# Kernel tuning notes

Hardware: AMD Instinct MI355X
Metric: run time of the kernel (lower is better)

## Reference

```python
import jax, jax.numpy as jnp
import numpy as np

B, N, D, Q, H = 8, 2048, 64, 16, 2
C = 2 * D + 1          # combined dim = 129
C8 = C // 8            # per-head qk dim = 16
K = 8192               # number of observed nodes
NEG = -9.0e15


def setup_inputs() -> dict:
    key = jax.random.key(0)
    ks = jax.random.split(key, 18)
    s = 0.05
    inp = {
        "x": jax.random.normal(ks[0], (B, N, D + 1), jnp.float32),
        "h": jax.random.normal(ks[1], (B, N, D), jnp.float32),
        "query_vectors": jax.random.normal(ks[2], (K, Q), jnp.float32),
        "adj": jax.random.randint(ks[3], (B, N, N), 0, 2, jnp.int32),
        "nodes_flat": jnp.arange(K, dtype=jnp.int32),
        # per-head attention projections (jax convention: x @ W + b)
        "Wq": jax.random.normal(ks[4], (H, C, C8), jnp.float32) * s,
        "bq": jax.random.normal(ks[5], (H, C8), jnp.float32) * s,
        "Wk": jax.random.normal(ks[6], (H, C, C8), jnp.float32) * s,
        "bk": jax.random.normal(ks[7], (H, C8), jnp.float32) * s,
        "Wv": jax.random.normal(ks[8], (H, C, C), jnp.float32) * s,
        "bv": jax.random.normal(ks[9], (H, C), jnp.float32) * s,
        # hypernetwork MLP_Param weights for reset / update / candidate gates
        "W_r": jax.random.normal(ks[10], (Q, C, D), jnp.float32) * s,
        "b_r": jax.random.normal(ks[11], (Q, D), jnp.float32) * s,
        "W_u": jax.random.normal(ks[12], (Q, C, D), jnp.float32) * s,
        "b_u": jax.random.normal(ks[13], (Q, D), jnp.float32) * s,
        "W_c": jax.random.normal(ks[14], (Q, C, D), jnp.float32) * s,
        "b_c": jax.random.normal(ks[15], (Q, D), jnp.float32) * s,
    }
    return inp


def _gate(x_sel, qv, W, b):
    # MLP_Param: W_n = einsum('nd,dio->nio', qv, W); out = x @ W_n + qv @ b
    # contract the combined dim first to avoid the [K, C, D] intermediate
    t = jnp.einsum('kc,qco->kqo', x_sel, W)      # [K, Q, D]
    return jnp.einsum('kq,kqo->ko', qv, t) + qv @ b


def reference(x, h, query_vectors, adj, nodes_flat,
              Wq, bq, Wk, bk, Wv, bv,
              W_r, b_r, W_u, b_u, W_c, b_c):
    combined = jnp.concatenate([x, h], axis=-1)                 # [B, N, C]
    q = jnp.einsum('bnc,hcd->hbnd', combined, Wq) + bq[:, None, None, :]
    k = jnp.einsum('bnc,hcd->hbnd', combined, Wk) + bk[:, None, None, :]
    v = jnp.einsum('bnc,hcd->hbnd', combined, Wv) + bv[:, None, None, :]
    scores = jnp.einsum('hbnd,hbmd->hbnm', q, k) / jnp.sqrt(jnp.float32(C8))
    scores = jax.nn.leaky_relu(scores, 0.2)
    scores = jnp.where(adj[None] == 0, NEG, scores)
    attn = jax.nn.softmax(scores, axis=-1)                      # [H, B, N, N]
    h_prime = jnp.einsum('hbnm,hbmc->hbnc', attn, v)
    comb_attn = h_prime.mean(axis=0)                            # [B, N, C]

    sel = comb_attn.reshape(-1, C)[nodes_flat]                  # [K, C]
    r = jax.nn.sigmoid(_gate(sel, query_vectors, W_r, b_r))     # [K, D]
    u = jax.nn.sigmoid(_gate(sel, query_vectors, W_u, b_u))     # [K, D]

    h_flat = h.reshape(-1, D)
    h_sel = r * h_flat[nodes_flat]                              # r * h[nodes_ind]
    h_flat = h_flat.at[nodes_flat].set(h_sel)
    h_new = h_flat.reshape(h.shape)

    comb_new = jnp.concatenate([x, h_new], axis=-1)             # [B, N, C]
    sel2 = comb_new.reshape(-1, C)[nodes_flat]
    cand = jnp.tanh(_gate(sel2, query_vectors, W_c, b_c))       # [K, D]

    return (1.0 - u) * h_sel + u * cand                         # [K, D]
```

## Files before the change

### kernel.cpp

```cpp
#include <hip/hip_runtime.h>
#include <hip/hip_bf16.h>


typedef _Float16 h2_t __attribute__((ext_vector_type(2)));
typedef _Float16 h8_t __attribute__((ext_vector_type(8)));
typedef float    f4_t __attribute__((ext_vector_type(4)));
#define MFMA16x32(a,b,c) __builtin_amdgcn_mfma_f32_16x16x32_f16(a,b,c,0,0,0)

#define OB_QG    0
#define OB_KG    524288
#define OB_VT    1048576
#define OB_MASK  5767168
#define OB_WALL  7864320
#define OB_HACC  7971840
#define OB_LSUM  16622592
#define OB_WTRU  16688128
#define OB_WTC   17253376

__global__ __launch_bounds__(256) void pack_adj(const int* __restrict__ adj,
                                                unsigned* __restrict__ mask) {
    long tg = (long)blockIdx.x * 256 + threadIdx.x;
    for (int it = 0; it < 32; ++it) {
        long i = tg + (long)it * 524288;
        int a = adj[i];
        unsigned long long bal = __ballot(a != 0);
        if ((threadIdx.x & 63) == 0)
            *(unsigned long long*)(mask + (i >> 5)) = bal;
    }
}

__global__ __launch_bounds__(256) void repack_all(
    const float* __restrict__ Wq, const float* __restrict__ bq,
    const float* __restrict__ Wk, const float* __restrict__ bk,
    const float* __restrict__ Wv, const float* __restrict__ bv,
    const float* __restrict__ Wr, const float* __restrict__ br,
    const float* __restrict__ Wu, const float* __restrict__ bu,
    const float* __restrict__ Wc, const float* __restrict__ bc,
    _Float16* __restrict__ Wall, _Float16* __restrict__ WtRu,
    _Float16* __restrict__ WtC) {
    int idx = blockIdx.x * 256 + threadIdx.x;
    if (idx < 6720) {
        int ct = idx / 320;
        int rem = idx % 320;
        int s = rem >> 6, lane = rem & 63;
        int n = ct * 16 + (lane & 15);
        int quad = lane >> 4;
        int h2 = (n >= 164) ? 1 : 0;
        int nn = n - h2 * 164;
        h8_t v;
        #pragma unroll
        for (int j = 0; j < 8; ++j) {
            int k = s * 32 + quad * 8 + j;
            float f = 0.f;
            if (n < 328) {
                if (nn < 16) {
                    if (k < 129)       f = Wq[(h2 * 129 + k) * 16 + nn];
                    else if (k == 129) f = bq[h2 * 16 + nn];
                } else if (nn < 32) {
                    int d = nn - 16;
                    if (k < 129)       f = Wk[(h2 * 129 + k) * 16 + d];
                    else if (k == 129) f = bk[h2 * 16 + d];
                } else {
                    int vc = nn - 32;
                    if (vc < 129) {
                        if (k < 129)       f = Wv[(h2 * 129 + k) * 129 + vc];
                        else if (k == 129) f = bv[h2 * 129 + vc];
                    }
                }
            }
            v[j] = (_Float16)f;
        }
        *(h8_t*)(Wall + (size_t)idx * 8) = v;
    } else if (idx < 6720 + 35328) {
        int i2 = idx - 6720;
        int s = i2 / 512;
        int rem = i2 % 512;
        int ct = rem >> 6, lane = rem & 63;
        int o = ct * 16 + (lane & 15);
        int quad = lane >> 4;
        const float* W = (o < 64) ? Wr : Wu;
        const float* bb = (o < 64) ? br : bu;
        int oc = o & 63;
        h8_t v;
        #pragma unroll
        for (int j = 0; j < 8; ++j) {
            int kk = s * 32 + quad * 8 + j;
            float f = 0.f;
            if (kk < 2176) {
                int q = kk / 136, c = kk % 136;
                if (c < 129) f = W[(q * 129 + c) * 64 + oc];
            } else if (kk < 2192) {
                f = bb[(kk - 2176) * 64 + oc];
            }
            v[j] = (_Float16)f;
        }
        *(h8_t*)(WtRu + (size_t)i2 * 8) = v;
    } else if (idx < 59712) {
        int i2 = idx - 6720 - 35328;
        int s = i2 / 256;
        int rem = i2 % 256;
        int ct = rem >> 6, lane = rem & 63;
        int o = ct * 16 + (lane & 15);
        int quad = lane >> 4;
        h8_t v;
        #pragma unroll
        for (int j = 0; j < 8; ++j) {
            int kk = s * 32 + quad * 8 + j;
            float f = 0.f;
            if (kk < 2176) {
                int q = kk / 136, c = kk % 136;
                if (c < 129) f = Wc[(q * 129 + c) * 64 + o];
            } else if (kk < 2192) {
                f = bc[(kk - 2176) * 64 + o];
            }
            v[j] = (_Float16)f;
        }
        *(h8_t*)(WtC + (size_t)i2 * 8) = v;
    }
}

__global__ __launch_bounds__(256) void qkv_mfma(
    const float* __restrict__ x, const float* __restrict__ h,
    const _Float16* __restrict__ Wall,
    _Float16* __restrict__ qg, _Float16* __restrict__ kg,
    _Float16* __restrict__ vT) {
    __shared__ _Float16 at[16 * 168];
    __shared__ _Float16 vls[264 * 16];
    int t = threadIdx.x;
    int row0 = blockIdx.x * 16;
    for (int idx = t; idx < 16 * 160; idx += 256) {
        int r = idx / 160, c = idx % 160;
        int grow = row0 + r;
        float v = 0.f;
        if (c < 65)       v = x[grow * 65 + c];
        else if (c < 129) v = h[grow * 64 + (c - 65)];
        else if (c == 129) v = 1.0f;
        at[r * 168 + c] = (_Float16)v;
    }
    __syncthreads();
    int lane = t & 63, w = t >> 6;
    int l16 = lane & 15, quad = lane >> 4;
    for (int ct = w; ct < 21; ct += 4) {
        f4_t acc; acc[0]=0.f; acc[1]=0.f; acc[2]=0.f; acc[3]=0.f;
        int n = ct * 16 + l16;
        const _Float16* wp = Wall + ((size_t)ct * 320 + lane) * 8;
        #pragma unroll
        for (int s = 0; s < 5; ++s) {
            h8_t a = *(const h8_t*)(at + l16 * 168 + s * 32 + quad * 8);
            h8_t b = *(const h8_t*)(wp + (size_t)s * 512);
            acc = MFMA16x32(a, b, acc);
        }
        if (n < 328) {
            int h2 = (n >= 164) ? 1 : 0;
            int nn = n - h2 * 164;
            #pragma unroll
            for (int r = 0; r < 4; ++r) {
                int row = quad * 4 + r;
                _Float16 v = (_Float16)acc[r];
                if (nn < 16)      qg[(h2 * 8192 + row0 + row) * 16 + nn] = v;
                else if (nn < 32) kg[(h2 * 8192 + row0 + row) * 16 + (nn - 16)] = v;
                else              vls[(h2 * 132 + (nn - 32)) * 16 + row] = v;
            }
        }
    }
    __syncthreads();
    for (int idx = t; idx < 528; idx += 256) {
        int col = idx >> 1, half = idx & 1;
        int h2 = (col >= 132) ? 1 : 0;
        int cc = col - h2 * 132;
        uint4 v = ((const uint4*)vls)[idx];
        *(uint4*)(vT + ((size_t)(h2 * 144 + cc)) * 8192 + row0 + half * 8) = v;
    }
}

__global__ __launch_bounds__(256) void attn_fused(
    const _Float16* __restrict__ qg, const _Float16* __restrict__ kg,
    const _Float16* __restrict__ vT, const unsigned* __restrict__ mask,
    float* __restrict__ hacc, float* __restrict__ lsum, int tps) {
    __shared__ _Float16 vsm[144 * 88];
    __shared__ _Float16 pT[4 * 16 * 88];
    int t = threadIdx.x;
    int pid = blockIdx.x + 32 * (blockIdx.y + 8 * blockIdx.z);
    int xcd = pid & 7, j = pid >> 3;
    int nt = j & 31, hb = xcd, sp = j >> 5;
    int h2 = hb >> 2, b = hb & 3;
    int base = h2 * 8192 + b * 2048;
    int n0 = nt * 64;
    int lane = t & 63, w = t >> 6;
    int l16 = lane & 15, q = lane >> 4;
    int qrow = n0 + w * 16 + l16;
    _Float16* pTw = pT + w * 16 * 88;
    h8_t zero8;
    #pragma unroll
    for (int i = 0; i < 8; ++i) zero8[i] = (_Float16)0.f;
    h8_t qf = zero8;
    if (q < 2) qf = *(const h8_t*)(qg + (base + qrow) * 16 + 8 * q);
    const unsigned* mrw = mask + (b * 2048 + qrow) * 64;
    f4_t acc[9];
    #pragma unroll
    for (int i = 0; i < 9; ++i) { acc[i][0]=0.f; acc[i][1]=0.f; acc[i][2]=0.f; acc[i][3]=0.f; }
    float l_run = 0.f;

    int c0 = t >> 3, ch0 = t & 7;
    const _Float16* vsrc = vT + ((size_t)h2 * 144) * 8192 + b * 2048 + ch0 * 8;
    int mt0 = sp * tps, mtE = sp * tps + tps;

    uint4 rv0, rv1, rv2, rv3, rv4;
    h8_t kpre[4];
    uint2 mpre;
    {
        int m0 = mt0 * 64;
        rv0 = *(const uint4*)(vsrc + (size_t)(c0      ) * 8192 + m0);
        rv1 = *(const uint4*)(vsrc + (size_t)(c0 + 32 ) * 8192 + m0);
        rv2 = *(const uint4*)(vsrc + (size_t)(c0 + 64 ) * 8192 + m0);
        rv3 = *(const uint4*)(vsrc + (size_t)(c0 + 96 ) * 8192 + m0);
        if (t < 128) rv4 = *(const uint4*)(vsrc + (size_t)(c0 + 128) * 8192 + m0);
        #pragma unroll
        for (int ct = 0; ct < 4; ++ct) {
            kpre[ct] = zero8;
            if (q < 2)
                kpre[ct] = *(const h8_t*)(kg + (base + m0 + 16 * ct + l16) * 16 + 8 * q);
        }
        mpre = *(const uint2*)(mrw + (m0 >> 5));
    }

    for (int mt = mt0; mt < mtE; ++mt) {
        int m0 = mt * 64;
        __syncthreads();
        *(uint4*)(vsm + (c0      ) * 88 + ch0 * 8) = rv0;
        *(uint4*)(vsm + (c0 + 32 ) * 88 + ch0 * 8) = rv1;
        *(uint4*)(vsm + (c0 + 64 ) * 88 + ch0 * 8) = rv2;
        *(uint4*)(vsm + (c0 + 96 ) * 88 + ch0 * 8) = rv3;
        if (t < 128) *(uint4*)(vsm + (c0 + 128) * 88 + ch0 * 8) = rv4;
        __syncthreads();
        h8_t kf[4];
        #pragma unroll
        for (int ct = 0; ct < 4; ++ct) kf[ct] = kpre[ct];
        uint2 mw = mpre;
        if (mt + 1 < mtE) {
            int m1 = m0 + 64;
            rv0 = *(const uint4*)(vsrc + (size_t)(c0      ) * 8192 + m1);
            rv1 = *(const uint4*)(vsrc + (size_t)(c0 + 32 ) * 8192 + m1);
            rv2 = *(const uint4*)(vsrc + (size_t)(c0 + 64 ) * 8192 + m1);
            rv3 = *(const uint4*)(vsrc + (size_t)(c0 + 96 ) * 8192 + m1);
            if (t < 128) rv4 = *(const uint4*)(vsrc + (size_t)(c0 + 128) * 8192 + m1);
            #pragma unroll
            for (int ct = 0; ct < 4; ++ct) {
                kpre[ct] = zero8;
                if (q < 2)
                    kpre[ct] = *(const h8_t*)(kg + (base + m1 + 16 * ct + l16) * 16 + 8 * q);
            }
            mpre = *(const uint2*)(mrw + (m1 >> 5));
        }
        f4_t st[4];
        #pragma unroll
        for (int ct = 0; ct < 4; ++ct) {
            f4_t z4; z4[0]=0.f; z4[1]=0.f; z4[2]=0.f; z4[3]=0.f;
            st[ct] = MFMA16x32(kf[ct], qf, z4);
        }
        #pragma unroll
        for (int ct = 0; ct < 4; ++ct) {
            unsigned wb = (ct < 2) ? mw.x : mw.y;
            float p[4];
            #pragma unroll
            for (int r = 0; r < 4; ++r) {
                float sc = st[ct][r] * 0.25f;
                sc = sc > 0.f ? sc : 0.2f * sc;
                int bit = ((ct & 1) ? 16 : 0) + 4 * q + r;
                p[r] = ((wb >> bit) & 1u) ? __expf(sc) : 0.f;
                l_run += p[r];
            }
            h2_t p01; p01[0] = (_Float16)p[0]; p01[1] = (_Float16)p[1];
            h2_t p23; p23[0] = (_Float16)p[2]; p23[1] = (_Float16)p[3];
            *(h2_t*)(pTw + l16 * 88 + 16 * ct + 4 * q)     = p01;
            *(h2_t*)(pTw + l16 * 88 + 16 * ct + 4 * q + 2) = p23;
        }
        #pragma unroll
        for (int kh = 0; kh < 2; ++kh) {
            h8_t ap = *(const h8_t*)(pTw + l16 * 88 + 32 * kh + 8 * q);
            #pragma unroll
            for (int nb = 0; nb < 9; ++nb) {
                h8_t vf = *(const h8_t*)(vsm + (16 * nb + l16) * 88 + 32 * kh + 8 * q);
                acc[nb] = MFMA16x32(ap, vf, acc[nb]);
            }
        }
    }
    l_run += __shfl_xor(l_run, 16);
    l_run += __shfl_xor(l_run, 32);
    float* hc = hacc + (size_t)h2 * 8192 * 132;
    if (q == 0)
        atomicAdd(lsum + h2 * 8192 + b * 2048 + n0 + w * 16 + l16, l_run);
    #pragma unroll
    for (int nb = 0; nb < 9; ++nb) {
        int vc = 16 * nb + l16;
        if (vc < 132) {
            #pragma unroll
            for (int r = 0; r < 4; ++r) {
                int grow = b * 2048 + n0 + w * 16 + 4 * q + r;
                atomicAdd(hc + grow * 132 + vc, acc[nb][r]);
            }
        }
    }
}

__global__ __launch_bounds__(256) void gate_fused(
    const float* __restrict__ hacc, const float* __restrict__ lsum,
    const int* __restrict__ nodes, const float* __restrict__ qv,
    const _Float16* __restrict__ WtRu, const _Float16* __restrict__ WtC,
    const float* __restrict__ hbuf, const float* __restrict__ x,
    float* __restrict__ out) {
    __shared__ _Float16 selh[16 * 152];
    __shared__ _Float16 selh2[16 * 152];
    __shared__ float qvs[16 * 17];
    __shared__ float invl[32];
    __shared__ float hslds[16 * 66];
    __shared__ float ulds[16 * 66];
    int t = threadIdx.x;
    int k0 = blockIdx.x * 16;
    if (t < 32) {
        int r = t >> 1, hh = t & 1;
        int grow = nodes[k0 + r];
        invl[t] = 0.5f / lsum[hh * 8192 + grow];
    }
    __syncthreads();
    for (int idx = t; idx < 16 * 136; idx += 256) {
        int r = idx / 136, c = idx % 136;
        _Float16 v = (_Float16)0.f;
        if (c < 132) {
            int grow = nodes[k0 + r];
            v = (_Float16)(hacc[grow * 132 + c] * invl[r * 2] +
                           hacc[8192 * 132 + grow * 132 + c] * invl[r * 2 + 1]);
        }
        selh[r * 152 + c] = v;
    }
    for (int idx = t; idx < 16 * 136; idx += 256) {
        int r = idx / 136, c = idx % 136;
        _Float16 v = (_Float16)0.f;
        if (c < 65) v = (_Float16)x[nodes[k0 + r] * 65 + c];
        selh2[r * 152 + c] = v;
    }
    if (t < 256) {
        int r = t >> 4, q = t & 15;
        qvs[r * 17 + q] = qv[(k0 + r) * 16 + q];
    }
    __syncthreads();
    int lane = t & 63, w = t >> 6;
    int l16 = lane & 15, quad = lane >> 4;
    f4_t acc0, acc1;
    acc0[0]=0.f;acc0[1]=0.f;acc0[2]=0.f;acc0[3]=0.f;
    acc1[0]=0.f;acc1[1]=0.f;acc1[2]=0.f;acc1[3]=0.f;
    const _Float16* wp0 = WtRu + ((size_t)(2 * w) * 64 + lane) * 8;
    const _Float16* wp1 = wp0 + 512;
    for (int step = 0; step < 69; ++step) {
        h8_t a;
        if (step < 68) {
            int chunk = 4 * step + quad;
            int q = chunk / 17;
            int c0 = (chunk - q * 17) * 8;
            h8_t s8 = *(const h8_t*)(selh + l16 * 152 + c0);
            _Float16 qh = (_Float16)qvs[l16 * 17 + q];
            #pragma unroll
            for (int j = 0; j < 8; ++j) a[j] = s8[j] * qh;
        } else {
            int kl = quad * 8;
            #pragma unroll
            for (int j = 0; j < 8; ++j) {
                int kq = kl + j;
                a[j] = (kq < 16) ? (_Float16)qvs[l16 * 17 + kq] : (_Float16)0.f;
            }
        }
        h8_t b0 = *(const h8_t*)(wp0 + (size_t)step * 4096);
        h8_t b1 = *(const h8_t*)(wp1 + (size_t)step * 4096);
        acc0 = MFMA16x32(a, b0, acc0);
        acc1 = MFMA16x32(a, b1, acc1);
    }
    #pragma unroll
    for (int tt = 0; tt < 2; ++tt) {
        f4_t ac = tt ? acc1 : acc0;
        int o = (2 * w + tt) * 16 + l16;
        #pragma unroll
        for (int r = 0; r < 4; ++r) {
            int row = quad * 4 + r;
            float sg = 1.f / (1.f + __expf(-ac[r]));
            if (o < 64) {
                float hs = sg * hbuf[nodes[k0 + row] * 64 + o];
                hslds[row * 66 + o] = hs;
                selh2[row * 152 + 65 + o] = (_Float16)hs;
            } else {
                ulds[row * 66 + (o - 64)] = sg;
            }
        }
    }
    if (t < 112) {
        int r = t / 7, c = 129 + (t % 7);
        selh2[r * 152 + c] = (_Float16)0.f;
    }
    __syncthreads();
    f4_t acc2;
    acc2[0]=0.f;acc2[1]=0.f;acc2[2]=0.f;acc2[3]=0.f;
    const _Float16* wp = WtC + ((size_t)w * 64 + lane) * 8;
    for (int step = 0; step < 69; ++step) {
        h8_t a;
        if (step < 68) {
            int chunk = 4 * step + quad;
            int q = chunk / 17;
            int c0 = (chunk - q * 17) * 8;
            h8_t s8 = *(const h8_t*)(selh2 + l16 * 152 + c0);
            _Float16 qh = (_Float16)qvs[l16 * 17 + q];
            #pragma unroll
            for (int j = 0; j < 8; ++j) a[j] = s8[j] * qh;
        } else {
            int kl = quad * 8;
            #pragma unroll
            for (int j = 0; j < 8; ++j) {
                int kq = kl + j;
                a[j] = (kq < 16) ? (_Float16)qvs[l16 * 17 + kq] : (_Float16)0.f;
            }
        }
        h8_t b = *(const h8_t*)(wp + (size_t)step * 2048);
        acc2 = MFMA16x32(a, b, acc2);
    }
    int o = w * 16 + l16;
    #pragma unroll
    for (int r = 0; r < 4; ++r) {
        int row = quad * 4 + r;
        float cv = tanhf(acc2[r]);
        float hs = hslds[row * 66 + o];
        float uv = ulds[row * 66 + o];
        out[(k0 + row) * 64 + o] = (1.f - uv) * hs + uv * cv;
    }
}

extern "C" void kernel_launch(void* const* d_in, const int* in_sizes, int n_in,
                              void* d_out, int out_size, void* d_ws, size_t ws_size,
                              hipStream_t stream) {
    const float* x   = (const float*)d_in[0];
    const float* h   = (const float*)d_in[1];
    const float* qv  = (const float*)d_in[2];
    const int*   adj = (const int*)d_in[3];
    const int*   nod = (const int*)d_in[4];
    const float* Wq  = (const float*)d_in[5];
    const float* bq  = (const float*)d_in[6];
    const float* Wk  = (const float*)d_in[7];
    const float* bk  = (const float*)d_in[8];
    const float* Wv  = (const float*)d_in[9];
    const float* bv  = (const float*)d_in[10];
    const float* Wr  = (const float*)d_in[11];
    const float* br  = (const float*)d_in[12];
    const float* Wu  = (const float*)d_in[13];
    const float* bu  = (const float*)d_in[14];
    const float* Wc  = (const float*)d_in[15];
    const float* bc  = (const float*)d_in[16];

    char* wsb = (char*)d_ws;
    _Float16* qg   = (_Float16*)(wsb + OB_QG);
    _Float16* kg   = (_Float16*)(wsb + OB_KG);
    _Float16* vT   = (_Float16*)(wsb + OB_VT);
    unsigned* mask = (unsigned*)(wsb + OB_MASK);
    _Float16* Wall = (_Float16*)(wsb + OB_WALL);
    float* hacc    = (float*)(wsb + OB_HACC);
    float* lsum    = (float*)(wsb + OB_LSUM);
    _Float16* WtRu = (_Float16*)(wsb + OB_WTRU);
    _Float16* WtC  = (_Float16*)(wsb + OB_WTC);

    pack_adj<<<dim3(2048), 256, 0, stream>>>(adj, mask);
    repack_all<<<dim3(234), 256, 0, stream>>>(Wq, bq, Wk, bk, Wv, bv,
                                              Wr, br, Wu, bu, Wc, bc,
                                              Wall, WtRu, WtC);
    qkv_mfma<<<dim3(512), 256, 0, stream>>>(x, h, Wall, qg, kg, vT);
    hipMemsetAsync(hacc, 0, (size_t)8650752 + 65536, stream);
    attn_fused<<<dim3(32, 8, 4), 256, 0, stream>>>(qg, kg, vT, mask,
                                                   hacc, lsum, 8);
    gate_fused<<<dim3(512), 256, 0, stream>>>(hacc, lsum, nod, qv,
                                              WtRu, WtC, h, x,
                                              (float*)d_out);
}
```

Baseline: 343.9 us.

## Load V tiles directly into LDS with XOR-swizzled layout

Replaces the register-staged V tile copy (global load into registers, then an LDS store) with direct global-to-LDS loads via global_load_lds into an unpadded, XOR-swizzled 64-column layout. The LDS reads are rewritten to match the swizzle, and the sync points are rearranged so the next tile's load is issued after the PV MFMAs. MFMA priority is raised around the PV loop. This is meant to cut VGPR pressure and LDS-store instructions, but the next V tile is no longer prefetched during compute, so less latency may be hidden.

New measurement: 344.9 us. No clear change (+0.3%).

```diff
diff --git a/kernel.cpp b/kernel.cpp
--- a/kernel.cpp
+++ b/kernel.cpp
@@ -177,7 +177,7 @@
     const _Float16* __restrict__ qg, const _Float16* __restrict__ kg,
     const _Float16* __restrict__ vT, const unsigned* __restrict__ mask,
     float* __restrict__ hacc, float* __restrict__ lsum, int tps) {
-    __shared__ _Float16 vsm[144 * 88];
+    __shared__ _Float16 vsm[144 * 64];
     __shared__ _Float16 pT[4 * 16 * 88];
     int t = threadIdx.x;
     int pid = blockIdx.x + 32 * (blockIdx.y + 8 * blockIdx.z);
@@ -201,20 +201,19 @@
     for (int i = 0; i < 9; ++i) { acc[i][0]=0.f; acc[i][1]=0.f; acc[i][2]=0.f; acc[i][3]=0.f; }
     float l_run = 0.f;
 
-    int c0 = t >> 3, ch0 = t & 7;
-    const _Float16* vsrc = vT + ((size_t)h2 * 144) * 8192 + b * 2048 + ch0 * 8;
+    int vcol_l = (lane >> 3);
+    int kch_l  = (lane & 7) ^ vcol_l;
+    const _Float16* vtb = vT + (size_t)h2 * 144 * 8192 + b * 2048 + 8 * kch_l;
     int mt0 = sp * tps, mtE = sp * tps + tps;
 
-    uint4 rv0, rv1, rv2, rv3, rv4;
     h8_t kpre[4];
     uint2 mpre;
     {
         int m0 = mt0 * 64;
-        rv0 = *(const uint4*)(vsrc + (size_t)(c0      ) * 8192 + m0);
-        rv1 = *(const uint4*)(vsrc + (size_t)(c0 + 32 ) * 8192 + m0);
-        rv2 = *(const uint4*)(vsrc + (size_t)(c0 + 64 ) * 8192 + m0);
-        rv3 = *(const uint4*)(vsrc + (size_t)(c0 + 96 ) * 8192 + m0);
-        if (t < 128) rv4 = *(const uint4*)(vsrc + (size_t)(c0 + 128) * 8192 + m0);
+        for (int jj = w; jj < 18; jj += 4)
+            __builtin_amdgcn_global_load_lds(
+                (const void*)(vtb + (size_t)(8 * jj + vcol_l) * 8192 + m0),
+                (void*)(vsm + jj * 512), 16, 0, 0);
         #pragma unroll
         for (int ct = 0; ct < 4; ++ct) {
             kpre[ct] = zero8;
@@ -225,33 +224,10 @@
     }
 
     for (int mt = mt0; mt < mtE; ++mt) {
-        int m0 = mt * 64;
-        __syncthreads();
-        *(uint4*)(vsm + (c0      ) * 88 + ch0 * 8) = rv0;
-        *(uint4*)(vsm + (c0 + 32 ) * 88 + ch0 * 8) = rv1;
-        *(uint4*)(vsm + (c0 + 64 ) * 88 + ch0 * 8) = rv2;
-        *(uint4*)(vsm + (c0 + 96 ) * 88 + ch0 * 8) = rv3;
-        if (t < 128) *(uint4*)(vsm + (c0 + 128) * 88 + ch0 * 8) = rv4;
-        __syncthreads();
         h8_t kf[4];
         #pragma unroll
         for (int ct = 0; ct < 4; ++ct) kf[ct] = kpre[ct];
         uint2 mw = mpre;
-        if (mt + 1 < mtE) {
-            int m1 = m0 + 64;
-            rv0 = *(const uint4*)(vsrc + (size_t)(c0      ) * 8192 + m1);
-            rv1 = *(const uint4*)(vsrc + (size_t)(c0 + 32 ) * 8192 + m1);
-            rv2 = *(const uint4*)(vsrc + (size_t)(c0 + 64 ) * 8192 + m1);
-            rv3 = *(const uint4*)(vsrc + (size_t)(c0 + 96 ) * 8192 + m1);
-            if (t < 128) rv4 = *(const uint4*)(vsrc + (size_t)(c0 + 128) * 8192 + m1);
-            #pragma unroll
-            for (int ct = 0; ct < 4; ++ct) {
-                kpre[ct] = zero8;
-                if (q < 2)
-                    kpre[ct] = *(const h8_t*)(kg + (base + m1 + 16 * ct + l16) * 16 + 8 * q);
-            }
-            mpre = *(const uint2*)(mrw + (m1 >> 5));
-        }
         f4_t st[4];
         #pragma unroll
         for (int ct = 0; ct < 4; ++ct) {
@@ -275,14 +251,37 @@
             *(h2_t*)(pTw + l16 * 88 + 16 * ct + 4 * q)     = p01;
             *(h2_t*)(pTw + l16 * 88 + 16 * ct + 4 * q + 2) = p23;
         }
+        __syncthreads();
+        if (mt + 1 < mtE) {
+            int m1 = (mt + 1) * 64;
+            #pragma unroll
+            for (int ct = 0; ct < 4; ++ct) {
+                kpre[ct] = zero8;
+                if (q < 2)
+                    kpre[ct] = *(const h8_t*)(kg + (base + m1 + 16 * ct + l16) * 16 + 8 * q);
+            }
+            mpre = *(const uint2*)(mrw + (m1 >> 5));
+        }
+        const char* vbb = (const char*)vsm;
+        __builtin_amdgcn_s_setprio(1);
         #pragma unroll
         for (int kh = 0; kh < 2; ++kh) {
             h8_t ap = *(const h8_t*)(pTw + l16 * 88 + 32 * kh + 8 * q);
+            int xsw = (((kh << 2) + q) ^ (l16 & 7)) << 4;
             #pragma unroll
             for (int nb = 0; nb < 9; ++nb) {
-                h8_t vf = *(const h8_t*)(vsm + (16 * nb + l16) * 88 + 32 * kh + 8 * q);
+                h8_t vf = *(const h8_t*)(vbb + ((16 * nb + l16) << 7) + xsw);
                 acc[nb] = MFMA16x32(ap, vf, acc[nb]);
             }
+        }
+        __builtin_amdgcn_s_setprio(0);
+        __syncthreads();
+        if (mt + 1 < mtE) {
+            int m1 = (mt + 1) * 64;
+            for (int jj = w; jj < 18; jj += 4)
+                __builtin_amdgcn_global_load_lds(
+                    (const void*)(vtb + (size_t)(8 * jj + vcol_l) * 8192 + m1),
+                    (void*)(vsm + jj * 512), 16, 0, 0);
         }
     }
     l_run += __shfl_xor(l_run, 16);
```
